# Performance work log

Hardware: AMD Instinct MI355X
Metric: run time of the kernel (lower is better)

## Reference

```python
import jax, jax.numpy as jnp
from jax import lax
import numpy as np

LAMBDA_DAG = 0.5
B, C = 64, 5000
PARENT_PROB = 0.0008  # ~4 parents per GO term


def setup_inputs() -> dict:
    key = jax.random.key(0)
    k1, k2, k3 = jax.random.split(key, 3)
    logits = jax.random.normal(k1, (B, C), dtype=jnp.float32)
    # sparse multilabel targets (binary floats, like GO annotations)
    labels = (jax.random.uniform(k2, (B, C)) < 0.02).astype(jnp.float32)
    # sparse binary DAG adjacency: dag[i, j] = 1 if j is a parent of i
    dag = (jax.random.uniform(k3, (C, C)) < PARENT_PROB).astype(jnp.float32)
    dag = dag * (1.0 - jnp.eye(C, dtype=jnp.float32))  # no self-parents
    return {"logits": logits, "labels": labels, "dag_matrix": dag}


def reference(logits, labels, dag_matrix):
    # BCEWithLogitsLoss (mean): log(1 + exp(l)) - l * y, numerically stable
    bce = jnp.mean(jnp.logaddexp(0.0, logits) - logits * labels)

    probs = jax.nn.sigmoid(logits)                      # [B, C]
    mask = (dag_matrix > 0).astype(probs.dtype)          # [C, C]
    n_par = mask.sum(axis=1)                             # [C] parents per child

    # Accumulate sum over batch of relu(p_child - p_parent)^2 as a [C, C] matrix
    # via scan over the batch dim (keeps peak memory at one [C, C] tile).
    def body(acc, p):  # p: [C]
        d = jnp.maximum(p[:, None] - p[None, :], 0.0)
        return acc + d * d, None

    nterms = probs.shape[1]
    viol_sum, _ = lax.scan(body, jnp.zeros((nterms, nterms), probs.dtype), probs)

    # per-child-term mean over (batch, n_parents_i), only for terms with parents
    per_term = (viol_sum * mask).sum(axis=1)             # [C]
    batch = jnp.asarray(probs.shape[0], probs.dtype)
    term_mean = jnp.where(n_par > 0, per_term / (batch * jnp.maximum(n_par, 1.0)), 0.0)

    total_edges = mask.sum()
    dag_penalty = jnp.where(total_edges > 0, term_mean.sum() / jnp.maximum(total_edges, 1.0), 0.0)

    loss = bce + LAMBDA_DAG * dag_penalty
    return loss
```

## Files before the change

### kernel.cpp

```cpp
#include <hip/hip_runtime.h>
#include <math.h>

#define LAMBDA_DAG 0.5f
#define SCAN_U 8
#define TILEN (256 * SCAN_U)
#define LBUF_CAP 2048

typedef float f4v __attribute__((ext_vector_type(4)));

__device__ __forceinline__ void process_edge_inline(
        unsigned e, const float* __restrict__ pT,
        float* __restrict__ per_term, float* __restrict__ npar, int B, int C) {
    const unsigned ui = e / (unsigned)C;
    const int i = (int)ui;
    const int j = (int)(e - ui * (unsigned)C);
    float s = 0.f;
    for (int b = 0; b < B; ++b) {
        float df = fmaxf(pT[(size_t)i * B + b] - pT[(size_t)j * B + b], 0.f);
        s += df * df;
    }
    atomicAdd(&per_term[i], s);
    atomicAdd(&npar[i], 1.f);
}

__device__ __forceinline__ f4v ld4nt(const float* p) {
    return __builtin_nontemporal_load((const f4v*)p);
}

#define PUSH_EDGE(E)                                                        \
    {                                                                       \
        const int pos = atomicAdd(&lcnt, 1);                                \
        if (pos < LBUF_CAP) lbuf[pos] = (E);                                \
        else if (pos < segw) seg[pos] = (E);                                \
        else if (inline_ok) process_edge_inline((E), pT, per_term, npar,    \
                                                B, C);                      \
    }

#define PROCESS_TILE(R, tbase)                                              \
    {                                                                       \
        unsigned any = 0u;                                                  \
        _Pragma("unroll")                                                   \
        for (int u = 0; u < SCAN_U; ++u)                                    \
            any |= __float_as_uint(R[u][0]) | __float_as_uint(R[u][1]) |    \
                   __float_as_uint(R[u][2]) | __float_as_uint(R[u][3]);     \
        if (any != 0u) {                                                    \
            _Pragma("unroll")                                               \
            for (int u = 0; u < SCAN_U; ++u) {                              \
                _Pragma("unroll")                                           \
                for (int k = 0; k < 4; ++k) {                               \
                    if (R[u][k] > 0.f) {                                    \
                        const unsigned e = (unsigned)(((tbase) + u * 256 +  \
                                           (int)threadIdx.x) * 4 + k);      \
                        PUSH_EDGE(e);                                       \
                    }                                                       \
                }                                                           \
            }                                                               \
        }                                                                   \
    }

__global__ void __launch_bounds__(256) k_main(
        const float* __restrict__ logits,
        const float* __restrict__ labels,
        const float* __restrict__ dag,
        float* __restrict__ pT,
        float* __restrict__ bce_part,
        float* __restrict__ per_term,
        float* __restrict__ npar,
        unsigned* __restrict__ elist,
        int* __restrict__ bcount,
        int segw, int inline_ok,
        int tb, int te,
        int sb_base, int sbN,
        int do_tails,
        int nbAx, int nbAy, int B, int C) {
    const int nbA = nbAx * nbAy;
    const int bid = blockIdx.x;
    const int tid = threadIdx.x;

    __shared__ float tile[64][17];
    __shared__ float sred[256];
    __shared__ unsigned lbuf[LBUF_CAP];
    __shared__ int lcnt;

    if (bid < nbA) {
        for (int i = bid * 256 + tid; i < C; i += nbA * 256) {
            per_term[i] = 0.f;
            npar[i] = 0.f;
        }
        const int bx = bid % nbAx, by = bid / nbAx;
        const int c0 = bx * 64;
        const int b0 = by * 16;
        const int rows = (B - b0 < 16) ? (B - b0) : 16;
        const int lc = tid & 63;
        const int c  = c0 + lc;
        const bool valid = (c < C);
        float acc = 0.f;
        if (rows > 0) {
            for (int r = tid >> 6; r < rows; r += 4) {
                const int b = b0 + r;
                float l = 0.f, y = 0.f;
                if (valid) {
                    l = logits[(size_t)b * C + c];
                    y = labels[(size_t)b * C + c];
                    acc += fmaxf(l, 0.f) + log1pf(expf(-fabsf(l))) - l * y;
                }
                tile[lc][r] = 1.f / (1.f + expf(-l));
            }
        }
        __syncthreads();
        if (rows > 0) {
            if ((rows & 3) == 0) {
                const int r4 = rows >> 2;
                const int tot = 64 * r4;
                for (int t = tid; t < tot; t += 256) {
                    const int row = t / r4;
                    const int q = t - row * r4;
                    const int c2 = c0 + row;
                    if (c2 < C) {
                        float4 v;
                        v.x = tile[row][q * 4 + 0];
                        v.y = tile[row][q * 4 + 1];
                        v.z = tile[row][q * 4 + 2];
                        v.w = tile[row][q * 4 + 3];
                        *(float4*)(pT + (size_t)c2 * B + b0 + q * 4) = v;
                    }
                }
            } else {
                const int tot = 64 * rows;
                for (int t = tid; t < tot; t += 256) {
                    const int row = t / rows;
                    const int r = t - row * rows;
                    const int c2 = c0 + row;
                    if (c2 < C) pT[(size_t)c2 * B + b0 + r] = tile[row][r];
                }
            }
        }
        sred[tid] = acc;
        __syncthreads();
        for (int s = 128; s > 0; s >>= 1) {
            if (tid < s) sred[tid] += sred[tid + s];
            __syncthreads();
        }
        if (tid == 0) bce_part[bid] = sred[0];
        return;
    }

    const int lsb = bid - nbA;
    const int sb  = sb_base + lsb;
    if (tid == 0) lcnt = 0;
    __syncthreads();
    unsigned* __restrict__ seg = elist + (size_t)sb * (size_t)segw;

    const int N  = C * C;
    const int N4 = N >> 2;
    const int NT = N4 / TILEN;
    const int span = (te > tb) ? ((te - tb) + sbN - 1) / sbN : 0;
    const int t0 = tb + lsb * span;
    const int t1 = (t0 + span < te) ? (t0 + span) : te;

    if (t0 < t1) {
        const float* p = dag + ((size_t)t0 * TILEN + tid) * 4;
        f4v a[SCAN_U], b[SCAN_U];
#pragma unroll
        for (int u = 0; u < SCAN_U; ++u) a[u] = ld4nt(p + u * 1024);
        for (int t = t0; t < t1; ++t) {
            const bool last = (t + 1 == t1);
            if (!last) {
#pragma unroll
                for (int u = 0; u < SCAN_U; ++u)
                    b[u] = ld4nt(p + TILEN * 4 + u * 1024);
            }
            PROCESS_TILE(a, t * TILEN);
            if (!last) {
#pragma unroll
                for (int u = 0; u < SCAN_U; ++u) a[u] = b[u];
            }
            p += TILEN * 4;
        }
    }

    if (do_tails) {
        for (int q = NT * TILEN + lsb * 256 + tid; q < N4; q += sbN * 256) {
            f4v d = ld4nt(dag + (size_t)q * 4);
#pragma unroll
            for (int k = 0; k < 4; ++k) {
                if (d[k] > 0.f) {
                    const unsigned e = (unsigned)(q * 4 + k);
                    PUSH_EDGE(e);
                }
            }
        }
        for (int e = (N4 << 2) + lsb * 256 + tid; e < N; e += sbN * 256) {
            if (dag[e] > 0.f) PUSH_EDGE((unsigned)e);
        }
    }

    __syncthreads();
    const int n  = lcnt;
    const int nl = (n < LBUF_CAP) ? n : LBUF_CAP;
    for (int t = tid; t < nl; t += 256)
        if (t < segw) seg[t] = lbuf[t];
    if (tid == 0) bcount[sb] = (n < segw) ? n : segw;
}

__global__ void __launch_bounds__(256) k_edges(
        const float* __restrict__ pT,
        const unsigned* __restrict__ elist,
        const int* __restrict__ bcount, int segw, int nseg,
        float* __restrict__ per_term,
        float* __restrict__ npar,
        int B, int C) {
    const int lane = threadIdx.x & 63;
    const int w    = threadIdx.x >> 6;
    for (int sb = blockIdx.x; sb < nseg; sb += gridDim.x) {
        int n = bcount[sb];
        if (n > segw) n = segw;
        const unsigned* seg = elist + (size_t)sb * (size_t)segw;
        for (int t = w; t < n; t += 4) {
            const unsigned e = seg[t];
            const unsigned ui = e / (unsigned)C;
            const int i = (int)ui;
            const int j = (int)(e - ui * (unsigned)C);
            const float* pi = pT + (size_t)i * B;
            const float* pj = pT + (size_t)j * B;
            float s = 0.f;
            for (int b = lane; b < B; b += 64) {
                float df = fmaxf(pi[b] - pj[b], 0.f);
                s += df * df;
            }
#pragma unroll
            for (int off = 32; off > 0; off >>= 1) s += __shfl_down(s, off, 64);
            if (lane == 0) {
                atomicAdd(&per_term[i], s);
                atomicAdd(&npar[i], 1.f);
            }
        }
    }
}

__global__ void k_final(const float* __restrict__ per_term,
                        const float* __restrict__ npar,
                        const float* __restrict__ bce_part, int nb,
                        float* __restrict__ out, int B, int C) {
    float bs = 0.f, ps = 0.f, es = 0.f;
    for (int k = threadIdx.x; k < nb; k += blockDim.x) bs += bce_part[k];
    for (int i = threadIdx.x; i < C; i += blockDim.x) {
        float np = npar[i];
        es += np;
        if (np > 0.f) ps += per_term[i] / ((float)B * np);
    }
    __shared__ float s1[256], s2[256], s3[256];
    s1[threadIdx.x] = bs;
    s2[threadIdx.x] = ps;
    s3[threadIdx.x] = es;
    __syncthreads();
    for (int s = blockDim.x >> 1; s > 0; s >>= 1) {
        if (threadIdx.x < s) {
            s1[threadIdx.x] += s1[threadIdx.x + s];
            s2[threadIdx.x] += s2[threadIdx.x + s];
            s3[threadIdx.x] += s3[threadIdx.x + s];
        }
        __syncthreads();
    }
    if (threadIdx.x == 0) {
        float penalty = (s3[0] > 0.f) ? (s2[0] / s3[0]) : 0.f;
        out[0] = s1[0] / (float)(B * C) + LAMBDA_DAG * penalty;
    }
}

extern "C" void kernel_launch(void* const* d_in, const int* in_sizes, int n_in,
                              void* d_out, int out_size, void* d_ws, size_t ws_size,
                              hipStream_t stream) {
    const float* logits = (const float*)d_in[0];
    const float* labels = (const float*)d_in[1];
    const float* dag    = (const float*)d_in[2];
    float* out = (float*)d_out;

    const int C = (int)(sqrt((double)in_sizes[2]) + 0.5);
    const int B = in_sizes[0] / C;

    const int gridAx = (C + 63) / 64;
    const int gridAy = (B + 15) / 16;
    const int nbA = gridAx * gridAy;

    const int N4 = (C * C) >> 2;
    const int NT = N4 / TILEN;
    const int scanB = 2048;
    const int nseg = scanB;
    const int span = (NT > 0) ? (NT + scanB - 1) / scanB : 0;
    const long long segw_full = (long long)(span + 1) * TILEN * 4;

    float* ws       = (float*)d_ws;
    float* pT       = ws;
    float* per_term = pT + (size_t)C * B;
    float* nparw    = per_term + C;
    float* bce_part = nparw + C;
    int*   bcount   = (int*)(bce_part + nbA);
    unsigned* elist = (unsigned*)(bcount + nseg);

    const size_t base_words = (size_t)C * B + 2 * (size_t)C + nbA + nseg;
    const size_t ws_words = ws_size / 4;
    long long avail = (ws_words > base_words)
                    ? (long long)(ws_words - base_words) : 0;

    int fused, inline_ok, segw;
    if (avail >= segw_full * nseg) {
        fused = 1; inline_ok = 0;
        segw = (int)segw_full;
    } else {
        fused = 0; inline_ok = 1;
        long long sw = avail / nseg;
        if (sw > 0x7fffffffLL) sw = 0x7fffffffLL;
        segw = (int)(sw < 0 ? 0 : sw);
    }

    if (fused) {
        k_main<<<nbA + scanB, 256, 0, stream>>>(
            logits, labels, dag, pT, bce_part, per_term, nparw,
            elist, bcount, segw, 0,
            0, NT, 0, scanB, 1, gridAx, gridAy, B, C);
    } else {
        k_main<<<nbA, 256, 0, stream>>>(
            logits, labels, dag, pT, bce_part, per_term, nparw,
            elist, bcount, segw, 0,
            0, 0, 0, 1, 0, gridAx, gridAy, B, C);
        k_main<<<scanB, 256, 0, stream>>>(
            logits, labels, dag, pT, bce_part, per_term, nparw,
            elist, bcount, segw, inline_ok,
            0, NT, 0, scanB, 1, 0, 0, B, C);
    }

    k_edges<<<nseg, 256, 0, stream>>>(pT, elist, bcount, segw, nseg,
                                      per_term, nparw, B, C);
    k_final<<<1, 256, 0, stream>>>(per_term, nparw, bce_part, nbA, out, B, C);
}
```

Before: 167.7 us.

## Replace per-block edge segments with a single compacted global edge pool

Scan blocks now reserve space in one global edge list through an atomic counter instead of writing into fixed per-block segments. The edge kernel then walks a dense list with grid-strided warps, which balances work and drops the many empty segments. Scan blocks are halved to 1024, k_edges shrinks to 256 blocks, and logits and labels get nontemporal loads. This adds a memset launch and global atomic contention on the counter, and the edge order becomes nondeterministic.

```diff
diff --git a/kernel.cpp b/kernel.cpp
--- a/kernel.cpp
+++ b/kernel.cpp
@@ -26,14 +26,20 @@
 __device__ __forceinline__ f4v ld4nt(const float* p) {
     return __builtin_nontemporal_load((const f4v*)p);
 }
+__device__ __forceinline__ float ld1nt(const float* p) {
+    return __builtin_nontemporal_load(p);
+}
 
 #define PUSH_EDGE(E)                                                        \
     {                                                                       \
         const int pos = atomicAdd(&lcnt, 1);                                \
         if (pos < LBUF_CAP) lbuf[pos] = (E);                                \
-        else if (pos < segw) seg[pos] = (E);                                \
-        else if (inline_ok) process_edge_inline((E), pT, per_term, npar,    \
-                                                B, C);                      \
+        else {                                                              \
+            const int gp = atomicAdd(ecnt, 1);                              \
+            if (gp < pool_cap) elist[gp] = (E);                             \
+            else if (inline_ok) process_edge_inline((E), pT, per_term,      \
+                                                    npar, B, C);            \
+        }                                                                   \
     }
 
 #define PROCESS_TILE(R, tbase)                                              \
@@ -67,10 +73,10 @@
         float* __restrict__ per_term,
         float* __restrict__ npar,
         unsigned* __restrict__ elist,
-        int* __restrict__ bcount,
-        int segw, int inline_ok,
+        int* __restrict__ ecnt,
+        int pool_cap, int inline_ok,
         int tb, int te,
-        int sb_base, int sbN,
+        int sbN,
         int do_tails,
         int nbAx, int nbAy, int B, int C) {
     const int nbA = nbAx * nbAy;
@@ -100,8 +106,8 @@
                 const int b = b0 + r;
                 float l = 0.f, y = 0.f;
                 if (valid) {
-                    l = logits[(size_t)b * C + c];
-                    y = labels[(size_t)b * C + c];
+                    l = ld1nt(&logits[(size_t)b * C + c]);
+                    y = ld1nt(&labels[(size_t)b * C + c]);
                     acc += fmaxf(l, 0.f) + log1pf(expf(-fabsf(l))) - l * y;
                 }
                 tile[lc][r] = 1.f / (1.f + expf(-l));
@@ -146,10 +152,8 @@
     }
 
     const int lsb = bid - nbA;
-    const int sb  = sb_base + lsb;
     if (tid == 0) lcnt = 0;
     __syncthreads();
-    unsigned* __restrict__ seg = elist + (size_t)sb * (size_t)segw;
 
     const int N  = C * C;
     const int N4 = N >> 2;
@@ -196,44 +200,50 @@
     }
 
     __syncthreads();
+    __shared__ int gbase;
     const int n  = lcnt;
     const int nl = (n < LBUF_CAP) ? n : LBUF_CAP;
-    for (int t = tid; t < nl; t += 256)
-        if (t < segw) seg[t] = lbuf[t];
-    if (tid == 0) bcount[sb] = (n < segw) ? n : segw;
+    if (tid == 0) gbase = atomicAdd(ecnt, nl);
+    __syncthreads();
+    const int gb = gbase;
+    for (int t = tid; t < nl; t += 256) {
+        const int gp = gb + t;
+        if (gp < pool_cap) elist[gp] = lbuf[t];
+        else if (inline_ok) process_edge_inline(lbuf[t], pT, per_term,
+                                                npar, B, C);
+    }
 }
 
 __global__ void __launch_bounds__(256) k_edges(
         const float* __restrict__ pT,
         const unsigned* __restrict__ elist,
-        const int* __restrict__ bcount, int segw, int nseg,
+        const int* __restrict__ ecnt, int pool_cap,
         float* __restrict__ per_term,
         float* __restrict__ npar,
         int B, int C) {
+    int n = *ecnt;
+    if (n > pool_cap) n = pool_cap;
     const int lane = threadIdx.x & 63;
-    const int w    = threadIdx.x >> 6;
-    for (int sb = blockIdx.x; sb < nseg; sb += gridDim.x) {
-        int n = bcount[sb];
-        if (n > segw) n = segw;
-        const unsigned* seg = elist + (size_t)sb * (size_t)segw;
-        for (int t = w; t < n; t += 4) {
-            const unsigned e = seg[t];
-            const unsigned ui = e / (unsigned)C;
-            const int i = (int)ui;
-            const int j = (int)(e - ui * (unsigned)C);
-            const float* pi = pT + (size_t)i * B;
-            const float* pj = pT + (size_t)j * B;
-            float s = 0.f;
-            for (int b = lane; b < B; b += 64) {
-                float df = fmaxf(pi[b] - pj[b], 0.f);
-                s += df * df;
-            }
-#pragma unroll
-            for (int off = 32; off > 0; off >>= 1) s += __shfl_down(s, off, 64);
-            if (lane == 0) {
-                atomicAdd(&per_term[i], s);
-                atomicAdd(&npar[i], 1.f);
-            }
+    const int wid  = (blockIdx.x * blockDim.x + threadIdx.x) >> 6;
+    const int nw   = (gridDim.x * blockDim.x) >> 6;
+
+    for (int t = wid; t < n; t += nw) {
+        const unsigned e = elist[t];
+        const unsigned ui = e / (unsigned)C;
+        const int i = (int)ui;
+        const int j = (int)(e - ui * (unsigned)C);
+        const float* pi = pT + (size_t)i * B;
+        const float* pj = pT + (size_t)j * B;
+        float s = 0.f;
+        for (int b = lane; b < B; b += 64) {
+            float df = fmaxf(pi[b] - pj[b], 0.f);
+            s += df * df;
+        }
+#pragma unroll
+        for (int off = 32; off > 0; off >>= 1) s += __shfl_down(s, off, 64);
+        if (lane == 0) {
+            atomicAdd(&per_term[i], s);
+            atomicAdd(&npar[i], 1.f);
         }
     }
 }
@@ -285,52 +295,51 @@
 
     const int N4 = (C * C) >> 2;
     const int NT = N4 / TILEN;
-    const int scanB = 2048;
-    const int nseg = scanB;
-    const int span = (NT > 0) ? (NT + scanB - 1) / scanB : 0;
-    const long long segw_full = (long long)(span + 1) * TILEN * 4;
+    const int scanB = 1024;
 
     float* ws       = (float*)d_ws;
     float* pT       = ws;
     float* per_term = pT + (size_t)C * B;
     float* nparw    = per_term + C;
     float* bce_part = nparw + C;
-    int*   bcount   = (int*)(bce_part + nbA);
-    unsigned* elist = (unsigned*)(bcount + nseg);
-
-    const size_t base_words = (size_t)C * B + 2 * (size_t)C + nbA + nseg;
+    int*   ecnt     = (int*)(bce_part + nbA);
+    unsigned* elist = (unsigned*)(ecnt + 1);
+
+    const size_t base_words = (size_t)C * B + 2 * (size_t)C + nbA + 1;
     const size_t ws_words = ws_size / 4;
     long long avail = (ws_words > base_words)
                     ? (long long)(ws_words - base_words) : 0;
-
-    int fused, inline_ok, segw;
-    if (avail >= segw_full * nseg) {
+    const long long need = (long long)C * (long long)C;
+
+    int fused, inline_ok, pool_cap;
+    if (avail >= need) {
         fused = 1; inline_ok = 0;
-        segw = (int)segw_full;
+        pool_cap = (int)((need < 0x7fffffffLL) ? need : 0x7fffffffLL);
     } else {
         fused = 0; inline_ok = 1;
-        long long sw = avail / nseg;
-        if (sw > 0x7fffffffLL) sw = 0x7fffffffLL;
-        segw = (int)(sw < 0 ? 0 : sw);
-    }
+        pool_cap = (int)((avail < 0) ? 0
+                   : (avail > 0x7fffffffLL ? 0x7fffffffLL : avail));
+    }
+
+    hipMemsetAsync(ecnt, 0, sizeof(int), stream);
 
     if (fused) {
         k_main<<<nbA + scanB, 256, 0, stream>>>(
             logits, labels, dag, pT, bce_part, per_term, nparw,
-            elist, bcount, segw, 0,
-            0, NT, 0, scanB, 1, gridAx, gridAy, B, C);
+            elist, ecnt, pool_cap, 0,
+            0, NT, scanB, 1, gridAx, gridAy, B, C);
     } else {
         k_main<<<nbA, 256, 0, stream>>>(
             logits, labels, dag, pT, bce_part, per_term, nparw,
-            elist, bcount, segw, 0,
-            0, 0, 0, 1, 0, gridAx, gridAy, B, C);
+            elist, ecnt, pool_cap, 0,
+            0, 0, 1, 0, gridAx, gridAy, B, C);
         k_main<<<scanB, 256, 0, stream>>>(
             logits, labels, dag, pT, bce_part, per_term, nparw,
-            elist, bcount, segw, inline_ok,
-            0, NT, 0, scanB, 1, 0, 0, B, C);
-    }
-
-    k_edges<<<nseg, 256, 0, stream>>>(pT, elist, bcount, segw, nseg,
-                                      per_term, nparw, B, C);
+            elist, ecnt, pool_cap, inline_ok,
+            0, NT, scanB, 1, 0, 0, B, C);
+    }
+
+    k_edges<<<256, 256, 0, stream>>>(pT, elist, ecnt, pool_cap,
+                                     per_term, nparw, B, C);
     k_final<<<1, 256, 0, stream>>>(per_term, nparw, bce_part, nbA, out, B, C);
 }
```

Result: slower. 188.6 us (+12.5%).
